# Performance work log

Hardware: AMD Instinct MI355X
Metric: run time of the kernel (lower is better)

Reference implementation:

```python
import jax, jax.numpy as jnp
import numpy as np

NEG_SLOPE = 0.2
NUM_GRAPHS = 64


def _gatv2_layer(x, src, dst, Wl, bl, Wr, br, att, bias, n_nodes, heads, ch):
    # lin_l (source) and lin_r (target) transforms -> [N, H, C]
    xs = (x @ Wl + bl).reshape(n_nodes, heads, ch)
    xd = (x @ Wr + br).reshape(n_nodes, heads, ch)
    s = xs[src]                                   # [E, H, C] gathered source feats
    e = jax.nn.leaky_relu(s + xd[dst], NEG_SLOPE)  # GATv2: leaky_relu BEFORE att dot
    score = jnp.einsum('ehc,hc->eh', e, att)       # [E, H]
    # segment softmax over edges sharing the same target node
    smax = jax.ops.segment_max(score, dst, num_segments=n_nodes)
    ex = jnp.exp(score - smax[dst])
    denom = jax.ops.segment_sum(ex, dst, num_segments=n_nodes)
    alpha = ex / denom[dst]                        # [E, H]
    out = jax.ops.segment_sum(alpha[:, :, None] * s, dst, num_segments=n_nodes)
    return out.reshape(n_nodes, heads * ch) + bias


def setup_inputs() -> dict:
    key = jax.random.key(0)
    ks = jax.random.split(key, 20)
    N, E, F = 50000, 800000, 128
    H, C = 4, 64
    G = NUM_GRAPHS
    sc = 0.05
    inp = {
        'x': jax.random.normal(ks[0], (N, F), jnp.float32),
        'edge_index': jax.random.randint(ks[1], (2, E), 0, N, jnp.int64 if jax.config.read('jax_enable_x64') else jnp.int32).astype(jnp.int32),
        'batch': jnp.sort(jax.random.randint(ks[2], (N,), 0, G)).astype(jnp.int32),
        'W_l1': jax.random.normal(ks[3], (F, H * C)) * sc,
        'b_l1': jax.random.normal(ks[4], (H * C,)) * sc,
        'W_r1': jax.random.normal(ks[5], (F, H * C)) * sc,
        'b_r1': jax.random.normal(ks[6], (H * C,)) * sc,
        'att1': jax.random.normal(ks[7], (H, C)) * sc,
        'bias1': jax.random.normal(ks[8], (H * C,)) * sc,
        'W_l2': jax.random.normal(ks[9], (H * C, C)) * sc,
        'b_l2': jax.random.normal(ks[10], (C,)) * sc,
        'W_r2': jax.random.normal(ks[11], (H * C, C)) * sc,
        'b_r2': jax.random.normal(ks[12], (C,)) * sc,
        'att2': jax.random.normal(ks[13], (1, C)) * sc,
        'bias2': jax.random.normal(ks[14], (C,)) * sc,
        'W_lin': jax.random.normal(ks[15], (C, 1)) * sc,
        'b_lin': jax.random.normal(ks[16], (1,)) * sc,
    }
    return inp


def reference(x, edge_index, batch, W_l1, b_l1, W_r1, b_r1, att1, bias1,
              W_l2, b_l2, W_r2, b_r2, att2, bias2, W_lin, b_lin):
    N = x.shape[0]
    # PyG GATv2Conv adds self-loops by default
    loops = jnp.arange(N, dtype=edge_index.dtype)
    src = jnp.concatenate([edge_index[0], loops])
    dst = jnp.concatenate([edge_index[1], loops])

    h = _gatv2_layer(x, src, dst, W_l1, b_l1, W_r1, b_r1, att1, bias1, N, 4, 64)
    h = jax.nn.relu(h)  # dropout=identity (eval), norm=Identity
    h = _gatv2_layer(h, src, dst, W_l2, b_l2, W_r2, b_r2, att2, bias2, N, 1, 64)

    # global mean pool over graphs
    sums = jax.ops.segment_sum(h, batch, num_segments=NUM_GRAPHS)
    counts = jax.ops.segment_sum(jnp.ones((N,), h.dtype), batch, num_segments=NUM_GRAPHS)
    pooled = sums / jnp.maximum(counts, 1.0)[:, None]  # [G, 64]
    return pooled @ W_lin + b_lin                      # [G, 1]
```

## Files before the change

### kernel.cpp

```cpp
#include <hip/hip_runtime.h>
#include <hip/hip_bf16.h>
#include <math.h>

typedef __attribute__((ext_vector_type(8))) short short8;
typedef __attribute__((ext_vector_type(4))) float floatx4;

__device__ __forceinline__ float bf2f(unsigned short u) {
  union { unsigned int i; float f; } v; v.i = ((unsigned int)u) << 16; return v.f;
}
__device__ __forceinline__ unsigned short f2bf(float f) {
  union { float f; unsigned int u; } v; v.f = f;
  unsigned int r = (v.u + 0x7fffu + ((v.u >> 16) & 1u)) >> 16;
  return (unsigned short)r;
}
__device__ __forceinline__ int imin(int a, int b) { return a < b ? a : b; }
__device__ __forceinline__ int iclamp(int v, int lo, int hi) {
  return v < lo ? lo : (v > hi ? hi : v);
}
__device__ __forceinline__ float uasf(unsigned int u) {
  union { unsigned int i; float f; } v; v.i = u; return v.f;
}
__device__ __forceinline__ float sum16(float x) {
  union { float f; int i; } a, t;
  a.f = x;
  t.i = __builtin_amdgcn_update_dpp(0, a.i, 0x121, 0xF, 0xF, true); a.f += t.f;
  t.i = __builtin_amdgcn_update_dpp(0, a.i, 0x122, 0xF, 0xF, true); a.f += t.f;
  t.i = __builtin_amdgcn_update_dpp(0, a.i, 0x124, 0xF, 0xF, true); a.f += t.f;
  t.i = __builtin_amdgcn_update_dpp(0, a.i, 0x128, 0xF, 0xF, true); a.f += t.f;
  return a.f;
}

__global__ void k_sentinel(float* out, float val) {
  if (threadIdx.x < 64) out[threadIdx.x] = val;
}

struct CvtSegs {
  const void* src[10];
  unsigned short* dst[10];
  int len[10];
};

__global__ void k_prep(const void* __restrict__ x, unsigned short* __restrict__ x_c,
                       int n8, CvtSegs segs,
                       const void* __restrict__ s0, const void* __restrict__ s1,
                       const void* __restrict__ s2, const void* __restrict__ s3,
                       unsigned short* __restrict__ d0, unsigned short* __restrict__ d1,
                       unsigned short* __restrict__ d2, unsigned short* __restrict__ d3,
                       const int* __restrict__ edst, int* deg, int E, int N,
                       int* dflag, int* colx, int ET, int nCvt8, int nTransB) {
  __shared__ int csh;
  if (threadIdx.x == 0) csh = 0;
  __syncthreads();
  {
    unsigned short u = ((const unsigned short*)x)[threadIdx.x];
    int e = (u >> 7) & 0xFF;
    atomicAdd(&csh, (u == 0) || (e >= 100 && e <= 145));
  }
  __syncthreads();
  int isf = (csh < 240);

  int b = blockIdx.x;
  if (b < nCvt8) {
    if (!isf) return;
    int i = b * 256 + threadIdx.x;
    if (i >= n8) return;
    const float* s = (const float*)x + (size_t)i * 8;
    ushort4 a, c;
    a.x = f2bf(s[0]); a.y = f2bf(s[1]); a.z = f2bf(s[2]); a.w = f2bf(s[3]);
    c.x = f2bf(s[4]); c.y = f2bf(s[5]); c.z = f2bf(s[6]); c.w = f2bf(s[7]);
    ((ushort4*)x_c)[i * 2] = a;
    ((ushort4*)x_c)[i * 2 + 1] = c;
    return;
  }
  b -= nCvt8;
  if (b < 10) {
    if (b == 0) {
      if (threadIdx.x == 0) dflag[0] = isf;
      if (threadIdx.x >= 240) colx[ET + (threadIdx.x - 240)] = 0;
    }
    int i = threadIdx.x;
    if (i < segs.len[b])
      segs.dst[b][i] = isf ? f2bf(((const float*)segs.src[b])[i])
                           : ((const unsigned short*)segs.src[b])[i];
    return;
  }
  b -= 10;
  if (b < nTransB) {
    int idx = b * 256 + threadIdx.x;
    const void* src; unsigned short* dst; int R, C, loc;
    if (idx < 32768)      { src = s0; dst = d0; R = 128; C = 256; loc = idx; }
    else if (idx < 65536) { src = s1; dst = d1; R = 128; C = 256; loc = idx - 32768; }
    else if (idx < 81920) { src = s2; dst = d2; R = 256; C = 64;  loc = idx - 65536; }
    else                  { src = s3; dst = d3; R = 256; C = 64;  loc = idx - 81920; }
    unsigned short u = isf ? f2bf(((const float*)src)[loc])
                           : ((const unsigned short*)src)[loc];
    int r = loc / C, cc = loc - r * C;
    dst[cc * R + r] = u;
    return;
  }
  b -= nTransB;
  int base = b * 1024 + threadIdx.x;
#pragma unroll
  for (int k = 0; k < 4; ++k) {
    int e = base + k * 256;
    if (e < E) atomicAdd(&deg[iclamp(edst[e], 0, N - 1)], 1);
  }
}

__global__ __launch_bounds__(1024) void k_scan1(const int* __restrict__ deg, int* bsum, int N) {
  __shared__ int sm[1024];
  int tid = threadIdx.x;
  int i = blockIdx.x * 1024 + tid;
  sm[tid] = (i < N) ? deg[i] + 1 : 0;
  __syncthreads();
  for (int off = 512; off > 0; off >>= 1) {
    if (tid < off) sm[tid] += sm[tid + off];
    __syncthreads();
  }
  if (tid == 0) bsum[blockIdx.x] = sm[0];
}

__global__ __launch_bounds__(1024) void k_scan3(const int* __restrict__ deg,
                                                const int* __restrict__ bsum,
                                                int* rowptr, int* cursor, int N) {
  __shared__ int sm[1024];
  __shared__ int boff;
  int tid = threadIdx.x;
  if (tid == 0) {
    int r = 0;
    for (int b = 0; b < blockIdx.x; ++b) r += bsum[b];
    boff = r;
  }
  int i = blockIdx.x * 1024 + tid;
  int v = (i < N) ? deg[i] + 1 : 0;
  sm[tid] = v;
  __syncthreads();
  for (int off = 1; off < 1024; off <<= 1) {
    int t = (tid >= off) ? sm[tid - off] : 0;
    __syncthreads();
    sm[tid] += t;
    __syncthreads();
  }
  if (i < N) {
    int ex = sm[tid] - v + boff;
    rowptr[i] = ex;
    cursor[i] = ex;
    if (i == N - 1) rowptr[N] = ex + v;
  }
}

template <int K, int CT, int RT>
__device__ __forceinline__ void gemm2r_body(
    int bx, int by, int tid,
    const unsigned short* __restrict__ A,
    const unsigned short* __restrict__ BTl, const unsigned short* __restrict__ BTr,
    const unsigned short* __restrict__ bl, const unsigned short* __restrict__ br,
    unsigned short* __restrict__ outl, unsigned short* __restrict__ outr,
    int Nrows, int M) {
  constexpr int KI = K / 32;
  int lane = tid & 63;
  int wave = tid >> 6;
  int r = lane & 15, q = lane >> 4;
  int col0 = by * (4 * CT * 16) + wave * (CT * 16);
  int row0 = bx * (16 * RT);
  short8 Bl[KI][CT], Br[KI][CT];
#pragma unroll
  for (int t = 0; t < CT; ++t) {
    const unsigned short* bpl = BTl + (size_t)(col0 + t * 16 + r) * K + q * 8;
    const unsigned short* bpr = BTr + (size_t)(col0 + t * 16 + r) * K + q * 8;
#pragma unroll
    for (int k = 0; k < KI; ++k) {
      Bl[k][t] = *reinterpret_cast<const short8*>(bpl + k * 32);
      Br[k][t] = *reinterpret_cast<const short8*>(bpr + k * 32);
    }
  }
  float bvl[CT], bvr[CT];
#pragma unroll
  for (int t = 0; t < CT; ++t) {
    bvl[t] = bf2f(bl[col0 + t * 16 + r]);
    bvr[t] = bf2f(br[col0 + t * 16 + r]);
  }
  short8 a[KI], an[KI];
  {
    int ar0 = imin(row0 + r, Nrows - 1);
    const unsigned short* Ap = A + (size_t)ar0 * K + q * 8;
#pragma unroll
    for (int k = 0; k < KI; ++k) a[k] = *reinterpret_cast<const short8*>(Ap + k * 32);
  }
  for (int rt = 0; rt < RT; ++rt) {
    if (rt + 1 < RT) {
      int arn = imin(row0 + (rt + 1) * 16 + r, Nrows - 1);
      const unsigned short* Apn = A + (size_t)arn * K + q * 8;
#pragma unroll
      for (int k = 0; k < KI; ++k) an[k] = *reinterpret_cast<const short8*>(Apn + k * 32);
    }
    floatx4 accl[CT], accr[CT];
#pragma unroll
    for (int t = 0; t < CT; ++t) {
      accl[t] = (floatx4){0.f, 0.f, 0.f, 0.f};
      accr[t] = (floatx4){0.f, 0.f, 0.f, 0.f};
    }
#pragma unroll
    for (int k = 0; k < KI; ++k) {
#pragma unroll
      for (int t = 0; t < CT; ++t) {
        accl[t] = __builtin_amdgcn_mfma_f32_16x16x32_bf16(a[k], Bl[k][t], accl[t], 0, 0, 0);
        accr[t] = __builtin_amdgcn_mfma_f32_16x16x32_bf16(a[k], Br[k][t], accr[t], 0, 0, 0);
      }
    }
#pragma unroll
    for (int t = 0; t < CT; ++t) {
      int col = col0 + t * 16 + r;
#pragma unroll
      for (int rr = 0; rr < 4; ++rr) {
        int row = row0 + rt * 16 + q * 4 + rr;
        if (row < Nrows) {
          outl[(size_t)row * M + col] = f2bf(accl[t][rr] + bvl[t]);
          outr[(size_t)row * M + col] = f2bf(accr[t][rr] + bvr[t]);
        }
      }
    }
#pragma unroll
    for (int k = 0; k < KI; ++k) a[k] = an[k];
  }
}

__global__ __launch_bounds__(256) void k_phase1(
    const unsigned short* __restrict__ A0, const unsigned short* __restrict__ A1,
    const int* __restrict__ dflag,
    const unsigned short* __restrict__ BTl, const unsigned short* __restrict__ BTr,
    const unsigned short* __restrict__ bl, const unsigned short* __restrict__ br,
    unsigned short* __restrict__ outl, unsigned short* __restrict__ outr,
    int Nrows, int M, int nG, int nS,
    const int* __restrict__ esrc, const int* __restrict__ edst,
    const int* __restrict__ rowptr, int* cursor, int* colx, int E, int N) {
  int b = blockIdx.x;
  int m2 = 2 * imin(nG, nS);
  bool isG;
  int idx;
  if (b < m2) { isG = (b & 1) == 0; idx = b >> 1; }
  else        { isG = nG > nS;      idx = imin(nG, nS) + (b - m2); }
  if (isG) {
    const unsigned short* A = dflag[0] ? A1 : A0;
    gemm2r_body<128, 2, 8>(idx >> 1, idx & 1, threadIdx.x, A, BTl, BTr, bl, br,
                           outl, outr, Nrows, M);
    return;
  }
  int ET = E + N;
  int base = idx * 1024 + threadIdx.x;
#pragma unroll
  for (int k = 0; k < 4; ++k) {
    int e = base + k * 256;
    if (e < ET) {
      if (e < E) {
        int s = iclamp(esrc[e], 0, N - 1), d = iclamp(edst[e], 0, N - 1);
        int pos = atomicAdd(&cursor[d], 1);
        colx[iclamp(pos, 0, ET - 1)] = s;
      } else {
        int i = e - E;
        colx[rowptr[i + 1] - 1] = i;
      }
    }
  }
}

__global__ __launch_bounds__(256) void k_gemm2r_l2(
    const unsigned short* __restrict__ A,
    const unsigned short* __restrict__ BTl, const unsigned short* __restrict__ BTr,
    const unsigned short* __restrict__ bl, const unsigned short* __restrict__ br,
    unsigned short* __restrict__ outl, unsigned short* __restrict__ outr,
    int Nrows, int M) {
  gemm2r_body<256, 1, 4>(blockIdx.x, 0, threadIdx.x, A, BTl, BTr, bl, br,
                         outl, outr, Nrows, M);
}

#define UNPACK2(u, v0, v1, v2, v3)          \
  v0 = uasf(u.x << 16); v1 = uasf(u.x & 0xffff0000u); \
  v2 = uasf(u.y << 16); v3 = uasf(u.y & 0xffff0000u);

#define SCORE(q0, q1, q2, q3, p)                             \
  p = q0 * 0.6f;                                             \
  p = fmaf(q1, 0.6f, p); p = fmaf(q2, 0.6f, p); p = fmaf(q3, 0.6f, p); \
  p = fmaf(c0, fabsf(q0), p); p = fmaf(c1, fabsf(q1), p);    \
  p = fmaf(c2, fabsf(q2), p); p = fmaf(c3, fabsf(q3), p);

__global__ __launch_bounds__(256) void k_agg_h4(
    const int* __restrict__ rowptr, const int* __restrict__ colx,
    const unsigned short* __restrict__ xs, const unsigned short* __restrict__ xd,
    const unsigned short* __restrict__ att, const unsigned short* __restrict__ bias,
    unsigned short* __restrict__ hout, int N) {
  int lane = threadIdx.x & 63;
  int dst = (blockIdx.x * 256 + threadIdx.x) >> 6;
  if (dst >= N) return;
  int off = lane << 2;
  unsigned int off2 = (unsigned int)off * 2;
  const char* xsb = (const char*)xs;
  ushort4 au = *reinterpret_cast<const ushort4*>(att + off);
  ushort4 du = *reinterpret_cast<const ushort4*>(xd + (size_t)dst * 256 + off);
  float a0 = bf2f(au.x), a1 = bf2f(au.y), a2 = bf2f(au.z), a3 = bf2f(au.w);
  float d0 = bf2f(du.x), d1 = bf2f(du.y), d2 = bf2f(du.z), d3 = bf2f(du.w);
  float ad0 = a0 * d0, ad1 = a1 * d1, ad2 = a2 * d2, ad3 = a3 * d3;
  float c0 = copysignf(0.4f, a0), c1 = copysignf(0.4f, a1);
  float c2 = copysignf(0.4f, a2), c3 = copysignf(0.4f, a3);
  float l = 0.f, o0 = 0.f, o1 = 0.f, o2 = 0.f, o3 = 0.f;
  int beg = __builtin_amdgcn_readfirstlane(rowptr[dst]);
  int end = __builtin_amdgcn_readfirstlane(rowptr[dst + 1]);
  int p0 = colx[beg], p1 = colx[beg + 1], p2 = colx[beg + 2], p3 = colx[beg + 3];
  uint2 ua = *(const uint2*)(xsb + (((unsigned)p0 << 9) + off2));
  uint2 ub = *(const uint2*)(xsb + (((unsigned)p1 << 9) + off2));
  uint2 uc = *(const uint2*)(xsb + (((unsigned)p2 << 9) + off2));
  uint2 ud = *(const uint2*)(xsb + (((unsigned)p3 << 9) + off2));
  int q0 = 0, q1 = 0, q2 = 0, q3 = 0;
  if (beg + 4 < end) {
    q0 = colx[beg + 4]; q1 = colx[beg + 5]; q2 = colx[beg + 6]; q3 = colx[beg + 7];
  }
  for (int e = beg; e < end; e += 4) {
    uint2 na = ua, nb = ub, nc = uc, nd = ud;
    if (e + 4 < end) {
      na = *(const uint2*)(xsb + (((unsigned)q0 << 9) + off2));
      nb = *(const uint2*)(xsb + (((unsigned)q1 << 9) + off2));
      nc = *(const uint2*)(xsb + (((unsigned)q2 << 9) + off2));
      nd = *(const uint2*)(xsb + (((unsigned)q3 << 9) + off2));
    }
    if (e + 8 < end) {
      q0 = colx[e + 8]; q1 = colx[e + 9]; q2 = colx[e + 10]; q3 = colx[e + 11];
    }
    float va0, va1, va2, va3, vb0, vb1, vb2, vb3;
    float vc0, vc1, vc2, vc3, vd0, vd1, vd2, vd3;
    UNPACK2(ua, va0, va1, va2, va3)
    UNPACK2(ub, vb0, vb1, vb2, vb3)
    UNPACK2(uc, vc0, vc1, vc2, vc3)
    UNPACK2(ud, vd0, vd1, vd2, vd3)
    float qa0 = fmaf(a0, va0, ad0), qa1 = fmaf(a1, va1, ad1);
    float qa2 = fmaf(a2, va2, ad2), qa3 = fmaf(a3, va3, ad3);
    float qb0 = fmaf(a0, vb0, ad0), qb1 = fmaf(a1, vb1, ad1);
    float qb2 = fmaf(a2, vb2, ad2), qb3 = fmaf(a3, vb3, ad3);
    float qc0 = fmaf(a0, vc0, ad0), qc1 = fmaf(a1, vc1, ad1);
    float qc2 = fmaf(a2, vc2, ad2), qc3 = fmaf(a3, vc3, ad3);
    float qd0 = fmaf(a0, vd0, ad0), qd1 = fmaf(a1, vd1, ad1);
    float qd2 = fmaf(a2, vd2, ad2), qd3 = fmaf(a3, vd3, ad3);
    float pa, pb, pc, pd;
    SCORE(qa0, qa1, qa2, qa3, pa)
    SCORE(qb0, qb1, qb2, qb3, pb)
    SCORE(qc0, qc1, qc2, qc3, pc)
    SCORE(qd0, qd1, qd2, qd3, pd)
    pa = sum16(pa); pb = sum16(pb); pc = sum16(pc); pd = sum16(pd);
    pa = fminf(pa, 60.f);
    pb = (e + 1 < end) ? fminf(pb, 60.f) : -INFINITY;
    pc = (e + 2 < end) ? fminf(pc, 60.f) : -INFINITY;
    pd = (e + 3 < end) ? fminf(pd, 60.f) : -INFINITY;
    float wa = __expf(pa), wb = __expf(pb), wc = __expf(pc), wd = __expf(pd);
    l += (wa + wb) + (wc + wd);
    o0 = fmaf(wa, va0, o0); o0 = fmaf(wb, vb0, o0);
    o0 = fmaf(wc, vc0, o0); o0 = fmaf(wd, vd0, o0);
    o1 = fmaf(wa, va1, o1); o1 = fmaf(wb, vb1, o1);
    o1 = fmaf(wc, vc1, o1); o1 = fmaf(wd, vd1, o1);
    o2 = fmaf(wa, va2, o2); o2 = fmaf(wb, vb2, o2);
    o2 = fmaf(wc, vc2, o2); o2 = fmaf(wd, vd2, o2);
    o3 = fmaf(wa, va3, o3); o3 = fmaf(wb, vb3, o3);
    o3 = fmaf(wc, vc3, o3); o3 = fmaf(wd, vd3, o3);
    ua = na; ub = nb; uc = nc; ud = nd;
  }
  float rl = 1.0f / l;
  ushort4 bu = *reinterpret_cast<const ushort4*>(bias + off);
  ushort4 res;
  res.x = f2bf(fmaxf(fmaf(o0, rl, bf2f(bu.x)), 0.f));
  res.y = f2bf(fmaxf(fmaf(o1, rl, bf2f(bu.y)), 0.f));
  res.z = f2bf(fmaxf(fmaf(o2, rl, bf2f(bu.z)), 0.f));
  res.w = f2bf(fmaxf(fmaf(o3, rl, bf2f(bu.w)), 0.f));
  *reinterpret_cast<ushort4*>(hout + (size_t)dst * 256 + off) = res;
}

__global__ __launch_bounds__(256) void k_agg_h1(
    const int* __restrict__ rowptr, const int* __restrict__ colx,
    const unsigned short* __restrict__ xs, const unsigned short* __restrict__ xd,
    const unsigned short* __restrict__ att, const unsigned short* __restrict__ bias,
    float* __restrict__ hout, int N) {
  int lane = threadIdx.x & 63;
  int wid = (blockIdx.x * 256 + threadIdx.x) >> 6;
  int g = lane >> 4, sl = lane & 15;
  int dst = wid * 4 + g;
  bool valid = dst < N;
  int dsafe = valid ? dst : 0;
  int cb = sl << 2;
  unsigned int cb2 = (unsigned int)cb * 2;
  const char* xsb = (const char*)xs;
  ushort4 au = *reinterpret_cast<const ushort4*>(att + cb);
  ushort4 du = *reinterpret_cast<const ushort4*>(xd + (size_t)dsafe * 64 + cb);
  float a0 = bf2f(au.x), a1 = bf2f(au.y), a2 = bf2f(au.z), a3 = bf2f(au.w);
  float d0 = bf2f(du.x), d1 = bf2f(du.y), d2 = bf2f(du.z), d3 = bf2f(du.w);
  float ad0 = a0 * d0, ad1 = a1 * d1, ad2 = a2 * d2, ad3 = a3 * d3;
  float c0 = copysignf(0.4f, a0), c1 = copysignf(0.4f, a1);
  float c2 = copysignf(0.4f, a2), c3 = copysignf(0.4f, a3);
  float l = 0.f, o0 = 0.f, o1 = 0.f, o2 = 0.f, o3 = 0.f;
  int beg = valid ? rowptr[dst] : 0;
  int end = valid ? rowptr[dst + 1] : 0;
  if (end > beg) {
    int p0 = colx[beg], p1 = colx[beg + 1], p2 = colx[beg + 2], p3 = colx[beg + 3];
    uint2 ua = *(const uint2*)(xsb + (((unsigned)p0 << 7) + cb2));
    uint2 ub = *(const uint2*)(xsb + (((unsigned)p1 << 7) + cb2));
    uint2 uc = *(const uint2*)(xsb + (((unsigned)p2 << 7) + cb2));
    uint2 ud = *(const uint2*)(xsb + (((unsigned)p3 << 7) + cb2));
    int q0 = 0, q1 = 0, q2 = 0, q3 = 0;
    if (beg + 4 < end) {
      q0 = colx[beg + 4]; q1 = colx[beg + 5]; q2 = colx[beg + 6]; q3 = colx[beg + 7];
    }
    for (int e = beg; e < end; e += 4) {
      uint2 na = ua, nb = ub, nc = uc, nd = ud;
      if (e + 4 < end) {
        na = *(const uint2*)(xsb + (((unsigned)q0 << 7) + cb2));
        nb = *(const uint2*)(xsb + (((unsigned)q1 << 7) + cb2));
        nc = *(const uint2*)(xsb + (((unsigned)q2 << 7) + cb2));
        nd = *(const uint2*)(xsb + (((unsigned)q3 << 7) + cb2));
      }
      if (e + 8 < end) {
        q0 = colx[e + 8]; q1 = colx[e + 9]; q2 = colx[e + 10]; q3 = colx[e + 11];
      }
      float va0, va1, va2, va3, vb0, vb1, vb2, vb3;
      float vc0, vc1, vc2, vc3, vd0, vd1, vd2, vd3;
      UNPACK2(ua, va0, va1, va2, va3)
      UNPACK2(ub, vb0, vb1, vb2, vb3)
      UNPACK2(uc, vc0, vc1, vc2, vc3)
      UNPACK2(ud, vd0, vd1, vd2, vd3)
      float qa0 = fmaf(a0, va0, ad0), qa1 = fmaf(a1, va1, ad1);
      float qa2 = fmaf(a2, va2, ad2), qa3 = fmaf(a3, va3, ad3);
      float qb0 = fmaf(a0, vb0, ad0), qb1 = fmaf(a1, vb1, ad1);
      float qb2 = fmaf(a2, vb2, ad2), qb3 = fmaf(a3, vb3, ad3);
      float qc0 = fmaf(a0, vc0, ad0), qc1 = fmaf(a1, vc1, ad1);
      float qc2 = fmaf(a2, vc2, ad2), qc3 = fmaf(a3, vc3, ad3);
      float qd0 = fmaf(a0, vd0, ad0), qd1 = fmaf(a1, vd1, ad1);
      float qd2 = fmaf(a2, vd2, ad2), qd3 = fmaf(a3, vd3, ad3);
      float pa, pb, pc, pd;
      SCORE(qa0, qa1, qa2, qa3, pa)
      SCORE(qb0, qb1, qb2, qb3, pb)
      SCORE(qc0, qc1, qc2, qc3, pc)
      SCORE(qd0, qd1, qd2, qd3, pd)
      pa = sum16(pa); pb = sum16(pb); pc = sum16(pc); pd = sum16(pd);
      pa = fminf(pa, 60.f);
      pb = (e + 1 < end) ? fminf(pb, 60.f) : -INFINITY;
      pc = (e + 2 < end) ? fminf(pc, 60.f) : -INFINITY;
      pd = (e + 3 < end) ? fminf(pd, 60.f) : -INFINITY;
      float wa = __expf(pa), wb = __expf(pb), wc = __expf(pc), wd = __expf(pd);
      l += (wa + wb) + (wc + wd);
      o0 = fmaf(wa, va0, o0); o0 = fmaf(wb, vb0, o0);
      o0 = fmaf(wc, vc0, o0); o0 = fmaf(wd, vd0, o0);
      o1 = fmaf(wa, va1, o1); o1 = fmaf(wb, vb1, o1);
      o1 = fmaf(wc, vc1, o1); o1 = fmaf(wd, vd1, o1);
      o2 = fmaf(wa, va2, o2); o2 = fmaf(wb, vb2, o2);
      o2 = fmaf(wc, vc2, o2); o2 = fmaf(wd, vd2, o2);
      o3 = fmaf(wa, va3, o3); o3 = fmaf(wb, vb3, o3);
      o3 = fmaf(wc, vc3, o3); o3 = fmaf(wd, vd3, o3);
      ua = na; ub = nb; uc = nc; ud = nd;
    }
  }
  if (valid) {
    float rl = 1.0f / l;
    ushort4 bu = *reinterpret_cast<const ushort4*>(bias + cb);
    floatx4 res;
    res[0] = fmaf(o0, rl, bf2f(bu.x));
    res[1] = fmaf(o1, rl, bf2f(bu.y));
    res[2] = fmaf(o2, rl, bf2f(bu.z));
    res[3] = fmaf(o3, rl, bf2f(bu.w));
    *reinterpret_cast<floatx4*>(hout + (size_t)dst * 64 + cb) = res;
  }
}

__global__ __launch_bounds__(256) void k_pool(const float* __restrict__ h2,
                                              const int* __restrict__ batch,
                                              float* pool, int* cnt, int N) {
  int lane = threadIdx.x & 63;
  int wid = (blockIdx.x * 256 + threadIdx.x) >> 6;
  int n0 = wid * 32;
  if (n0 >= N) return;
  int nend = imin(n0 + 32, N);
  float acc = 0.f;
  int c = 0;
  int gcur = iclamp(batch[n0], 0, 63);
  for (int n = n0; n < nend; ++n) {
    int gg = iclamp(batch[n], 0, 63);
    if (gg != gcur) {
      atomicAdd(&pool[gcur * 64 + lane], acc);
      if (lane == 0) atomicAdd(&cnt[gcur], c);
      acc = 0.f; c = 0; gcur = gg;
    }
    acc += h2[(size_t)n * 64 + lane];
    c++;
  }
  atomicAdd(&pool[gcur * 64 + lane], acc);
  if (lane == 0) atomicAdd(&cnt[gcur], c);
}

__global__ void k_final(const float* __restrict__ pool, const int* __restrict__ cnt,
                        const unsigned short* __restrict__ Wlinc,
                        const unsigned short* __restrict__ blinc,
                        float* __restrict__ out) {
  int g = threadIdx.x;
  if (g >= 64) return;
  float inv = 1.f / fmaxf((float)cnt[g], 1.f);
  float s = 0.f;
  for (int c = 0; c < 64; ++c) s += pool[g * 64 + c] * bf2f(Wlinc[c]);
  out[g] = fmaf(s, inv, bf2f(blinc[0]));
}

extern "C" void kernel_launch(void* const* d_in, const int* in_sizes, int n_in,
                              void* d_out, int out_size, void* d_ws, size_t ws_size,
                              hipStream_t stream) {
  const void* x     = d_in[0];
  const int*  ei    = (const int*)d_in[1];
  const int*  batch = (const int*)d_in[2];
  const void* Wl1 = d_in[3];  const void* bl1 = d_in[4];
  const void* Wr1 = d_in[5];  const void* br1 = d_in[6];
  const void* att1 = d_in[7]; const void* bias1 = d_in[8];
  const void* Wl2 = d_in[9];  const void* bl2 = d_in[10];
  const void* Wr2 = d_in[11]; const void* br2 = d_in[12];
  const void* att2 = d_in[13]; const void* bias2 = d_in[14];
  const void* Wlin = d_in[15]; const void* blin = d_in[16];
  float* out = (float*)d_out;

  const int F = 128, HC = 256, C2 = 64;
  int N = in_sizes[0] / F;
  int E = in_sizes[1] / 2;
  int ET = E + N;
  const int* esrc = ei;
  const int* edst = ei + E;

  char* w = (char*)d_ws;
  auto alloc = [&](size_t bytes) {
    char* p = w;
    w += (bytes + 255) & ~(size_t)255;
    return p;
  };
  int* dflag  = (int*)alloc(4);
  int* rowptr = (int*)alloc((size_t)(N + 1) * 4);
  int* cursor = (int*)alloc((size_t)N * 4);
  int* bsum   = (int*)alloc(1024 * 4);
  int* colx   = (int*)alloc((size_t)(ET + 16) * 4);
  unsigned short* smallc = (unsigned short*)alloc(4096);
  unsigned short* Wl1T = (unsigned short*)alloc((size_t)F * HC * 2);
  unsigned short* Wr1T = (unsigned short*)alloc((size_t)F * HC * 2);
  unsigned short* Wl2T = (unsigned short*)alloc((size_t)HC * C2 * 2);
  unsigned short* Wr2T = (unsigned short*)alloc((size_t)HC * C2 * 2);
  int* deg    = (int*)alloc((size_t)N * 4);
  float* pool = (float*)alloc(64 * 64 * 4);
  int* cnt    = (int*)alloc(64 * 4);
  unsigned short* xs1  = (unsigned short*)alloc((size_t)N * HC * 2);
  unsigned short* xd1  = (unsigned short*)alloc((size_t)N * HC * 2);
  unsigned short* h1   = (unsigned short*)alloc((size_t)N * HC * 2);
  size_t required = (size_t)(w - (char*)d_ws);
  size_t zlen = (size_t)((char*)cnt + 256 - (char*)deg);

  unsigned short* x_c = h1;
  unsigned short* xs2 = xs1;
  unsigned short* xd2 = xs1 + (size_t)N * C2;
  float*          h2  = (float*)xd1;

  unsigned short* bl1c   = smallc + 0;
  unsigned short* br1c   = smallc + 256;
  unsigned short* att1c  = smallc + 512;
  unsigned short* bias1c = smallc + 768;
  unsigned short* bl2c   = smallc + 1024;
  unsigned short* br2c   = smallc + 1088;
  unsigned short* att2c  = smallc + 1152;
  unsigned short* bias2c = smallc + 1216;
  unsigned short* Wlinc  = smallc + 1280;
  unsigned short* blinc  = smallc + 1344;

  if (ws_size < required) {
    k_sentinel<<<1, 64, 0, stream>>>(out, 1000.f + (float)(ws_size >> 20));
    return;
  }

  hipMemsetAsync(deg, 0, zlen, stream);

  CvtSegs segs;
  const void* ssrc[10] = {bl1, br1, att1, bias1, bl2, br2, att2, bias2, Wlin, blin};
  unsigned short* sdst[10] = {bl1c, br1c, att1c, bias1c, bl2c, br2c, att2c, bias2c, Wlinc, blinc};
  int slen[10] = {256, 256, 256, 256, 64, 64, 64, 64, 64, 1};
  for (int i = 0; i < 10; ++i) { segs.src[i] = ssrc[i]; segs.dst[i] = sdst[i]; segs.len[i] = slen[i]; }
  int n8 = N * F / 8;
  int nCvt8 = (n8 + 255) / 256;
  int nTransB = (2 * F * HC + 2 * HC * C2 + 255) / 256;
  int nHist = (E + 1023) / 1024;
  k_prep<<<nCvt8 + 10 + nTransB + nHist, 256, 0, stream>>>(
      x, x_c, n8, segs, Wl1, Wr1, Wl2, Wr2, Wl1T, Wr1T, Wl2T, Wr2T,
      edst, deg, E, N, dflag, colx, ET, nCvt8, nTransB);

  int nb = (N + 1023) / 1024;
  k_scan1<<<nb, 1024, 0, stream>>>(deg, bsum, N);
  k_scan3<<<nb, 1024, 0, stream>>>(deg, bsum, rowptr, cursor, N);

  int nG = ((N + 127) / 128) * 2;
  int nS = (ET + 1023) / 1024;
  k_phase1<<<nG + nS, 256, 0, stream>>>(
      (const unsigned short*)x, x_c, dflag, Wl1T, Wr1T, bl1c, br1c, xs1, xd1,
      N, HC, nG, nS, esrc, edst, rowptr, cursor, colx, E, N);

  k_agg_h4<<<(N + 3) / 4, 256, 0, stream>>>(rowptr, colx, xs1, xd1, att1c, bias1c, h1, N);

  k_gemm2r_l2<<<(N + 63) / 64, 256, 0, stream>>>(h1, Wl2T, Wr2T, bl2c, br2c, xs2, xd2, N, C2);
  k_agg_h1<<<(N + 15) / 16, 256, 0, stream>>>(rowptr, colx, xs2, xd2, att2c, bias2c, h2, N);

  int pw = (N + 31) / 32;
  k_pool<<<(pw + 3) / 4, 256, 0, stream>>>(h2, batch, pool, cnt, N);
  k_final<<<1, 64, 0, stream>>>(pool, cnt, Wlinc, blinc, out);
}
```

Measured before the change: 331.5 us.

## Fuse layer-2 linear transforms into layer-1 aggregation epilogue via MFMA

The layer-1 attention aggregation kernel now keeps its four per-block output rows in shared memory. It then runs the layer-2 lin_l/lin_r projections with bf16 MFMA inside the same block, writing xs2/xd2 directly. This removes the separate layer-2 GEMM launch and the write and re-read of the 256-wide h1 activation through global memory. In exchange, every block re-reads both full layer-2 weight matrices, uses only 4 of 16 MFMA rows, and issues narrow 2-byte scattered output stores.

```diff
diff --git a/kernel.cpp b/kernel.cpp
--- a/kernel.cpp
+++ b/kernel.cpp
@@ -264,16 +264,6 @@
   }
 }
 
-__global__ __launch_bounds__(256) void k_gemm2r_l2(
-    const unsigned short* __restrict__ A,
-    const unsigned short* __restrict__ BTl, const unsigned short* __restrict__ BTr,
-    const unsigned short* __restrict__ bl, const unsigned short* __restrict__ br,
-    unsigned short* __restrict__ outl, unsigned short* __restrict__ outr,
-    int Nrows, int M) {
-  gemm2r_body<256, 1, 4>(blockIdx.x, 0, threadIdx.x, A, BTl, BTr, bl, br,
-                         outl, outr, Nrows, M);
-}
-
 #define UNPACK2(u, v0, v1, v2, v3)          \
   v0 = uasf(u.x << 16); v1 = uasf(u.x & 0xffff0000u); \
   v2 = uasf(u.y << 16); v3 = uasf(u.y & 0xffff0000u);
@@ -288,119 +278,38 @@
     const int* __restrict__ rowptr, const int* __restrict__ colx,
     const unsigned short* __restrict__ xs, const unsigned short* __restrict__ xd,
     const unsigned short* __restrict__ att, const unsigned short* __restrict__ bias,
-    unsigned short* __restrict__ hout, int N) {
+    const unsigned short* __restrict__ Wl2T, const unsigned short* __restrict__ Wr2T,
+    const unsigned short* __restrict__ bl2, const unsigned short* __restrict__ br2,
+    unsigned short* __restrict__ xs2, unsigned short* __restrict__ xd2, int N) {
+  __shared__ unsigned short tile[16 * 264];
   int lane = threadIdx.x & 63;
-  int dst = (blockIdx.x * 256 + threadIdx.x) >> 6;
-  if (dst >= N) return;
+  int wid = threadIdx.x >> 6;
+  int dstBase = blockIdx.x * 4;
+  int dst = dstBase + wid;
+  bool dvalid = dst < N;
   int off = lane << 2;
   unsigned int off2 = (unsigned int)off * 2;
   const char* xsb = (const char*)xs;
   ushort4 au = *reinterpret_cast<const ushort4*>(att + off);
-  ushort4 du = *reinterpret_cast<const ushort4*>(xd + (size_t)dst * 256 + off);
+  int dsafe = dvalid ? dst : 0;
+  ushort4 du = *reinterpret_cast<const ushort4*>(xd + (size_t)dsafe * 256 + off);
   float a0 = bf2f(au.x), a1 = bf2f(au.y), a2 = bf2f(au.z), a3 = bf2f(au.w);
   float d0 = bf2f(du.x), d1 = bf2f(du.y), d2 = bf2f(du.z), d3 = bf2f(du.w);
   float ad0 = a0 * d0, ad1 = a1 * d1, ad2 = a2 * d2, ad3 = a3 * d3;
   float c0 = copysignf(0.4f, a0), c1 = copysignf(0.4f, a1);
   float c2 = copysignf(0.4f, a2), c3 = copysignf(0.4f, a3);
   float l = 0.f, o0 = 0.f, o1 = 0.f, o2 = 0.f, o3 = 0.f;
-  int beg = __builtin_amdgcn_readfirstlane(rowptr[dst]);
-  int end = __builtin_amdgcn_readfirstlane(rowptr[dst + 1]);
-  int p0 = colx[beg], p1 = colx[beg + 1], p2 = colx[beg + 2], p3 = colx[beg + 3];
-  uint2 ua = *(const uint2*)(xsb + (((unsigned)p0 << 9) + off2));
-  uint2 ub = *(const uint2*)(xsb + (((unsigned)p1 << 9) + off2));
-  uint2 uc = *(const uint2*)(xsb + (((unsigned)p2 << 9) + off2));
-  uint2 ud = *(const uint2*)(xsb + (((unsigned)p3 << 9) + off2));
-  int q0 = 0, q1 = 0, q2 = 0, q3 = 0;
-  if (beg + 4 < end) {
-    q0 = colx[beg + 4]; q1 = colx[beg + 5]; q2 = colx[beg + 6]; q3 = colx[beg + 7];
-  }
-  for (int e = beg; e < end; e += 4) {
-    uint2 na = ua, nb = ub, nc = uc, nd = ud;
-    if (e + 4 < end) {
-      na = *(const uint2*)(xsb + (((unsigned)q0 << 9) + off2));
-      nb = *(const uint2*)(xsb + (((unsigned)q1 << 9) + off2));
-      nc = *(const uint2*)(xsb + (((unsigned)q2 << 9) + off2));
-      nd = *(const uint2*)(xsb + (((unsigned)q3 << 9) + off2));
-    }
-    if (e + 8 < end) {
-      q0 = colx[e + 8]; q1 = colx[e + 9]; q2 = colx[e + 10]; q3 = colx[e + 11];
-    }
-    float va0, va1, va2, va3, vb0, vb1, vb2, vb3;
-    float vc0, vc1, vc2, vc3, vd0, vd1, vd2, vd3;
-    UNPACK2(ua, va0, va1, va2, va3)
-    UNPACK2(ub, vb0, vb1, vb2, vb3)
-    UNPACK2(uc, vc0, vc1, vc2, vc3)
-    UNPACK2(ud, vd0, vd1, vd2, vd3)
-    float qa0 = fmaf(a0, va0, ad0), qa1 = fmaf(a1, va1, ad1);
-    float qa2 = fmaf(a2, va2, ad2), qa3 = fmaf(a3, va3, ad3);
-    float qb0 = fmaf(a0, vb0, ad0), qb1 = fmaf(a1, vb1, ad1);
-    float qb2 = fmaf(a2, vb2, ad2), qb3 = fmaf(a3, vb3, ad3);
-    float qc0 = fmaf(a0, vc0, ad0), qc1 = fmaf(a1, vc1, ad1);
-    float qc2 = fmaf(a2, vc2, ad2), qc3 = fmaf(a3, vc3, ad3);
-    float qd0 = fmaf(a0, vd0, ad0), qd1 = fmaf(a1, vd1, ad1);
-    float qd2 = fmaf(a2, vd2, ad2), qd3 = fmaf(a3, vd3, ad3);
-    float pa, pb, pc, pd;
-    SCORE(qa0, qa1, qa2, qa3, pa)
-    SCORE(qb0, qb1, qb2, qb3, pb)
-    SCORE(qc0, qc1, qc2, qc3, pc)
-    SCORE(qd0, qd1, qd2, qd3, pd)
-    pa = sum16(pa); pb = sum16(pb); pc = sum16(pc); pd = sum16(pd);
-    pa = fminf(pa, 60.f);
-    pb = (e + 1 < end) ? fminf(pb, 60.f) : -INFINITY;
-    pc = (e + 2 < end) ? fminf(pc, 60.f) : -INFINITY;
-    pd = (e + 3 < end) ? fminf(pd, 60.f) : -INFINITY;
-    float wa = __expf(pa), wb = __expf(pb), wc = __expf(pc), wd = __expf(pd);
-    l += (wa + wb) + (wc + wd);
-    o0 = fmaf(wa, va0, o0); o0 = fmaf(wb, vb0, o0);
-    o0 = fmaf(wc, vc0, o0); o0 = fmaf(wd, vd0, o0);
-    o1 = fmaf(wa, va1, o1); o1 = fmaf(wb, vb1, o1);
-    o1 = fmaf(wc, vc1, o1); o1 = fmaf(wd, vd1, o1);
-    o2 = fmaf(wa, va2, o2); o2 = fmaf(wb, vb2, o2);
-    o2 = fmaf(wc, vc2, o2); o2 = fmaf(wd, vd2, o2);
-    o3 = fmaf(wa, va3, o3); o3 = fmaf(wb, vb3, o3);
-    o3 = fmaf(wc, vc3, o3); o3 = fmaf(wd, vd3, o3);
-    ua = na; ub = nb; uc = nc; ud = nd;
-  }
-  float rl = 1.0f / l;
-  ushort4 bu = *reinterpret_cast<const ushort4*>(bias + off);
-  ushort4 res;
-  res.x = f2bf(fmaxf(fmaf(o0, rl, bf2f(bu.x)), 0.f));
-  res.y = f2bf(fmaxf(fmaf(o1, rl, bf2f(bu.y)), 0.f));
-  res.z = f2bf(fmaxf(fmaf(o2, rl, bf2f(bu.z)), 0.f));
-  res.w = f2bf(fmaxf(fmaf(o3, rl, bf2f(bu.w)), 0.f));
-  *reinterpret_cast<ushort4*>(hout + (size_t)dst * 256 + off) = res;
-}
-
-__global__ __launch_bounds__(256) void k_agg_h1(
-    const int* __restrict__ rowptr, const int* __restrict__ colx,
-    const unsigned short* __restrict__ xs, const unsigned short* __restrict__ xd,
-    const unsigned short* __restrict__ att, const unsigned short* __restrict__ bias,
-    float* __restrict__ hout, int N) {
-  int lane = threadIdx.x & 63;
-  int wid = (blockIdx.x * 256 + threadIdx.x) >> 6;
-  int g = lane >> 4, sl = lane & 15;
-  int dst = wid * 4 + g;
-  bool valid = dst < N;
-  int dsafe = valid ? dst : 0;
-  int cb = sl << 2;
-  unsigned int cb2 = (unsigned int)cb * 2;
-  const char* xsb = (const char*)xs;
-  ushort4 au = *reinterpret_cast<const ushort4*>(att + cb);
-  ushort4 du = *reinterpret_cast<const ushort4*>(xd + (size_t)dsafe * 64 + cb);
-  float a0 = bf2f(au.x), a1 = bf2f(au.y), a2 = bf2f(au.z), a3 = bf2f(au.w);
-  float d0 = bf2f(du.x), d1 = bf2f(du.y), d2 = bf2f(du.z), d3 = bf2f(du.w);
-  float ad0 = a0 * d0, ad1 = a1 * d1, ad2 = a2 * d2, ad3 = a3 * d3;
-  float c0 = copysignf(0.4f, a0), c1 = copysignf(0.4f, a1);
-  float c2 = copysignf(0.4f, a2), c3 = copysignf(0.4f, a3);
-  float l = 0.f, o0 = 0.f, o1 = 0.f, o2 = 0.f, o3 = 0.f;
-  int beg = valid ? rowptr[dst] : 0;
-  int end = valid ? rowptr[dst + 1] : 0;
+  int beg = 0, end = 0;
+  if (dvalid) {
+    beg = __builtin_amdgcn_readfirstlane(rowptr[dst]);
+    end = __builtin_amdgcn_readfirstlane(rowptr[dst + 1]);
+  }
   if (end > beg) {
     int p0 = colx[beg], p1 = colx[beg + 1], p2 = colx[beg + 2], p3 = colx[beg + 3];
-    uint2 ua = *(const uint2*)(xsb + (((unsigned)p0 << 7) + cb2));
-    uint2 ub = *(const uint2*)(xsb + (((unsigned)p1 << 7) + cb2));
-    uint2 uc = *(const uint2*)(xsb + (((unsigned)p2 << 7) + cb2));
-    uint2 ud = *(const uint2*)(xsb + (((unsigned)p3 << 7) + cb2));
+    uint2 ua = *(const uint2*)(xsb + (((unsigned)p0 << 9) + off2));
+    uint2 ub = *(const uint2*)(xsb + (((unsigned)p1 << 9) + off2));
+    uint2 uc = *(const uint2*)(xsb + (((unsigned)p2 << 9) + off2));
+    uint2 ud = *(const uint2*)(xsb + (((unsigned)p3 << 9) + off2));
     int q0 = 0, q1 = 0, q2 = 0, q3 = 0;
     if (beg + 4 < end) {
       q0 = colx[beg + 4]; q1 = colx[beg + 5]; q2 = colx[beg + 6]; q3 = colx[beg + 7];
@@ -408,10 +317,10 @@
     for (int e = beg; e < end; e += 4) {
       uint2 na = ua, nb = ub, nc = uc, nd = ud;
       if (e + 4 < end) {
-        na = *(const uint2*)(xsb + (((unsigned)q0 << 7) + cb2));
-        nb = *(const uint2*)(xsb + (((unsigned)q1 << 7) + cb2));
-        nc = *(const uint2*)(xsb + (((unsigned)q2 << 7) + cb2));
-        nd = *(const uint2*)(xsb + (((unsigned)q3 << 7) + cb2));
+        na = *(const uint2*)(xsb + (((unsigned)q0 << 9) + off2));
+        nb = *(const uint2*)(xsb + (((unsigned)q1 << 9) + off2));
+        nc = *(const uint2*)(xsb + (((unsigned)q2 << 9) + off2));
+        nd = *(const uint2*)(xsb + (((unsigned)q3 << 9) + off2));
       }
       if (e + 8 < end) {
         q0 = colx[e + 8]; q1 = colx[e + 9]; q2 = colx[e + 10]; q3 = colx[e + 11];
@@ -452,6 +361,133 @@
       o3 = fmaf(wc, vc3, o3); o3 = fmaf(wd, vd3, o3);
       ua = na; ub = nb; uc = nc; ud = nd;
     }
+    float rl = 1.0f / l;
+    ushort4 bu = *reinterpret_cast<const ushort4*>(bias + off);
+    ushort4 res;
+    res.x = f2bf(fmaxf(fmaf(o0, rl, bf2f(bu.x)), 0.f));
+    res.y = f2bf(fmaxf(fmaf(o1, rl, bf2f(bu.y)), 0.f));
+    res.z = f2bf(fmaxf(fmaf(o2, rl, bf2f(bu.z)), 0.f));
+    res.w = f2bf(fmaxf(fmaf(o3, rl, bf2f(bu.w)), 0.f));
+    *reinterpret_cast<ushort4*>(&tile[wid * 264 + off]) = res;
+  }
+  __syncthreads();
+  {
+    int r = lane & 15, q = lane >> 4;
+    const unsigned short* bpl = Wl2T + (size_t)(wid * 16 + r) * 256 + q * 8;
+    const unsigned short* bpr = Wr2T + (size_t)(wid * 16 + r) * 256 + q * 8;
+    floatx4 accl = {0.f, 0.f, 0.f, 0.f}, accr = {0.f, 0.f, 0.f, 0.f};
+    short8 af0 = *reinterpret_cast<const short8*>(&tile[r * 264 + q * 8]);
+    short8 bl0 = *reinterpret_cast<const short8*>(bpl);
+    short8 br0 = *reinterpret_cast<const short8*>(bpr);
+#pragma unroll
+    for (int k = 0; k < 8; ++k) {
+      short8 af1 = af0, bl1 = bl0, br1 = br0;
+      if (k < 7) {
+        af1 = *reinterpret_cast<const short8*>(&tile[r * 264 + (k + 1) * 32 + q * 8]);
+        bl1 = *reinterpret_cast<const short8*>(bpl + (k + 1) * 32);
+        br1 = *reinterpret_cast<const short8*>(bpr + (k + 1) * 32);
+      }
+      accl = __builtin_amdgcn_mfma_f32_16x16x32_bf16(af0, bl0, accl, 0, 0, 0);
+      accr = __builtin_amdgcn_mfma_f32_16x16x32_bf16(af0, br0, accr, 0, 0, 0);
+      af0 = af1; bl0 = bl1; br0 = br1;
+    }
+    if (q == 0) {
+      int col = wid * 16 + r;
+      float bvl = bf2f(bl2[col]);
+      float bvr = bf2f(br2[col]);
+#pragma unroll
+      for (int rr = 0; rr < 4; ++rr) {
+        int dd = dstBase + rr;
+        if (dd < N) {
+          xs2[(size_t)dd * 64 + col] = f2bf(accl[rr] + bvl);
+          xd2[(size_t)dd * 64 + col] = f2bf(accr[rr] + bvr);
+        }
+      }
+    }
+  }
+}
+
+__global__ __launch_bounds__(256) void k_agg_h1(
+    const int* __restrict__ rowptr, const int* __restrict__ colx,
+    const unsigned short* __restrict__ xs, const unsigned short* __restrict__ xd,
+    const unsigned short* __restrict__ att, const unsigned short* __restrict__ bias,
+    float* __restrict__ hout, int N) {
+  int lane = threadIdx.x & 63;
+  int wid = (blockIdx.x * 256 + threadIdx.x) >> 6;
+  int g = lane >> 4, sl = lane & 15;
+  int dst = wid * 4 + g;
+  bool valid = dst < N;
+  int dsafe = valid ? dst : 0;
+  int cb = sl << 2;
+  unsigned int cb2 = (unsigned int)cb * 2;
+  const char* xsb = (const char*)xs;
+  ushort4 au = *reinterpret_cast<const ushort4*>(att + cb);
+  ushort4 du = *reinterpret_cast<const ushort4*>(xd + (size_t)dsafe * 64 + cb);
+  float a0 = bf2f(au.x), a1 = bf2f(au.y), a2 = bf2f(au.z), a3 = bf2f(au.w);
+  float d0 = bf2f(du.x), d1 = bf2f(du.y), d2 = bf2f(du.z), d3 = bf2f(du.w);
+  float ad0 = a0 * d0, ad1 = a1 * d1, ad2 = a2 * d2, ad3 = a3 * d3;
+  float c0 = copysignf(0.4f, a0), c1 = copysignf(0.4f, a1);
+  float c2 = copysignf(0.4f, a2), c3 = copysignf(0.4f, a3);
+  float l = 0.f, o0 = 0.f, o1 = 0.f, o2 = 0.f, o3 = 0.f;
+  int beg = valid ? rowptr[dst] : 0;
+  int end = valid ? rowptr[dst + 1] : 0;
+  if (end > beg) {
+    int p0 = colx[beg], p1 = colx[beg + 1], p2 = colx[beg + 2], p3 = colx[beg + 3];
+    uint2 ua = *(const uint2*)(xsb + (((unsigned)p0 << 7) + cb2));
+    uint2 ub = *(const uint2*)(xsb + (((unsigned)p1 << 7) + cb2));
+    uint2 uc = *(const uint2*)(xsb + (((unsigned)p2 << 7) + cb2));
+    uint2 ud = *(const uint2*)(xsb + (((unsigned)p3 << 7) + cb2));
+    int q0 = 0, q1 = 0, q2 = 0, q3 = 0;
+    if (beg + 4 < end) {
+      q0 = colx[beg + 4]; q1 = colx[beg + 5]; q2 = colx[beg + 6]; q3 = colx[beg + 7];
+    }
+    for (int e = beg; e < end; e += 4) {
+      uint2 na = ua, nb = ub, nc = uc, nd = ud;
+      if (e + 4 < end) {
+        na = *(const uint2*)(xsb + (((unsigned)q0 << 7) + cb2));
+        nb = *(const uint2*)(xsb + (((unsigned)q1 << 7) + cb2));
+        nc = *(const uint2*)(xsb + (((unsigned)q2 << 7) + cb2));
+        nd = *(const uint2*)(xsb + (((unsigned)q3 << 7) + cb2));
+      }
+      if (e + 8 < end) {
+        q0 = colx[e + 8]; q1 = colx[e + 9]; q2 = colx[e + 10]; q3 = colx[e + 11];
+      }
+      float va0, va1, va2, va3, vb0, vb1, vb2, vb3;
+      float vc0, vc1, vc2, vc3, vd0, vd1, vd2, vd3;
+      UNPACK2(ua, va0, va1, va2, va3)
+      UNPACK2(ub, vb0, vb1, vb2, vb3)
+      UNPACK2(uc, vc0, vc1, vc2, vc3)
+      UNPACK2(ud, vd0, vd1, vd2, vd3)
+      float qa0 = fmaf(a0, va0, ad0), qa1 = fmaf(a1, va1, ad1);
+      float qa2 = fmaf(a2, va2, ad2), qa3 = fmaf(a3, va3, ad3);
+      float qb0 = fmaf(a0, vb0, ad0), qb1 = fmaf(a1, vb1, ad1);
+      float qb2 = fmaf(a2, vb2, ad2), qb3 = fmaf(a3, vb3, ad3);
+      float qc0 = fmaf(a0, vc0, ad0), qc1 = fmaf(a1, vc1, ad1);
+      float qc2 = fmaf(a2, vc2, ad2), qc3 = fmaf(a3, vc3, ad3);
+      float qd0 = fmaf(a0, vd0, ad0), qd1 = fmaf(a1, vd1, ad1);
+      float qd2 = fmaf(a2, vd2, ad2), qd3 = fmaf(a3, vd3, ad3);
+      float pa, pb, pc, pd;
+      SCORE(qa0, qa1, qa2, qa3, pa)
+      SCORE(qb0, qb1, qb2, qb3, pb)
+      SCORE(qc0, qc1, qc2, qc3, pc)
+      SCORE(qd0, qd1, qd2, qd3, pd)
+      pa = sum16(pa); pb = sum16(pb); pc = sum16(pc); pd = sum16(pd);
+      pa = fminf(pa, 60.f);
+      pb = (e + 1 < end) ? fminf(pb, 60.f) : -INFINITY;
+      pc = (e + 2 < end) ? fminf(pc, 60.f) : -INFINITY;
+      pd = (e + 3 < end) ? fminf(pd, 60.f) : -INFINITY;
+      float wa = __expf(pa), wb = __expf(pb), wc = __expf(pc), wd = __expf(pd);
+      l += (wa + wb) + (wc + wd);
+      o0 = fmaf(wa, va0, o0); o0 = fmaf(wb, vb0, o0);
+      o0 = fmaf(wc, vc0, o0); o0 = fmaf(wd, vd0, o0);
+      o1 = fmaf(wa, va1, o1); o1 = fmaf(wb, vb1, o1);
+      o1 = fmaf(wc, vc1, o1); o1 = fmaf(wd, vd1, o1);
+      o2 = fmaf(wa, va2, o2); o2 = fmaf(wb, vb2, o2);
+      o2 = fmaf(wc, vc2, o2); o2 = fmaf(wd, vd2, o2);
+      o3 = fmaf(wa, va3, o3); o3 = fmaf(wb, vb3, o3);
+      o3 = fmaf(wc, vc3, o3); o3 = fmaf(wd, vd3, o3);
+      ua = na; ub = nb; uc = nc; ud = nd;
+    }
   }
   if (valid) {
     float rl = 1.0f / l;
@@ -550,8 +586,8 @@
   size_t zlen = (size_t)((char*)cnt + 256 - (char*)deg);
 
   unsigned short* x_c = h1;
-  unsigned short* xs2 = xs1;
-  unsigned short* xd2 = xs1 + (size_t)N * C2;
+  unsigned short* xs2 = h1;
+  unsigned short* xd2 = h1 + (size_t)N * C2;
   float*          h2  = (float*)xd1;
 
   unsigned short* bl1c   = smallc + 0;
@@ -595,9 +631,9 @@
       (const unsigned short*)x, x_c, dflag, Wl1T, Wr1T, bl1c, br1c, xs1, xd1,
       N, HC, nG, nS, esrc, edst, rowptr, cursor, colx, E, N);
 
-  k_agg_h4<<<(N + 3) / 4, 256, 0, stream>>>(rowptr, colx, xs1, xd1, att1c, bias1c, h1, N);
-
-  k_gemm2r_l2<<<(N + 63) / 64, 256, 0, stream>>>(h1, Wl2T, Wr2T, bl2c, br2c, xs2, xd2, N, C2);
+  k_agg_h4<<<(N + 3) / 4, 256, 0, stream>>>(
+      rowptr, colx, xs1, xd1, att1c, bias1c, Wl2T, Wr2T, bl2c, br2c, xs2, xd2, N);
+
   k_agg_h1<<<(N + 15) / 16, 256, 0, stream>>>(rowptr, colx, xs2, xd2, att2c, bias2c, h2, N);
 
   int pw = (N + 31) / 32;
```

New measurement: 380.8 us. 14.9% more time.
